# Optimization experiments

Hardware: AMD Instinct MI355X
Metric: run time of the kernel (lower is better)

Reference implementation:

```python
import jax, jax.numpy as jnp
import numpy as np

MODEL_DIM = 768
EMB_DIM = 768
NUM_HEADS = 12
HEAD_DIM = MODEL_DIM // NUM_HEADS  # 64
B, S = 4, 1024
LN_EPS = 1e-12


def setup_inputs() -> dict:
    key = jax.random.key(0)
    ks = jax.random.split(key, 12)
    s_in = 1.0 / np.sqrt(EMB_DIM)
    s_dm = 1.0 / np.sqrt(MODEL_DIM)
    return {
        "x": jax.random.normal(ks[0], (B, S, EMB_DIM), dtype=jnp.float32),
        # stacked per-head projection weights, [H, E, Dh] (in, out layout)
        "Wq": jax.random.normal(ks[1], (NUM_HEADS, EMB_DIM, HEAD_DIM), dtype=jnp.float32) * s_in,
        "bq": jax.random.normal(ks[2], (NUM_HEADS, HEAD_DIM), dtype=jnp.float32) * 0.02,
        "Wk": jax.random.normal(ks[3], (NUM_HEADS, EMB_DIM, HEAD_DIM), dtype=jnp.float32) * s_in,
        "bk": jax.random.normal(ks[4], (NUM_HEADS, HEAD_DIM), dtype=jnp.float32) * 0.02,
        "Wv": jax.random.normal(ks[5], (NUM_HEADS, EMB_DIM, HEAD_DIM), dtype=jnp.float32) * s_in,
        "bv": jax.random.normal(ks[6], (NUM_HEADS, HEAD_DIM), dtype=jnp.float32) * 0.02,
        # output dense [Dm, Dm] (in, out) + bias
        "Wd": jax.random.normal(ks[7], (MODEL_DIM, MODEL_DIM), dtype=jnp.float32) * s_dm,
        "bd": jax.random.normal(ks[8], (MODEL_DIM,), dtype=jnp.float32) * 0.02,
        # LayerNorm affine params
        "gamma": jnp.ones((MODEL_DIM,), dtype=jnp.float32),
        "beta": jnp.zeros((MODEL_DIM,), dtype=jnp.float32),
    }


def reference(x, Wq, bq, Wk, bk, Wv, bv, Wd, bd, gamma, beta):
    # Batched per-head projections: [B,S,E] x [H,E,Dh] -> [B,H,S,Dh]
    Q = jnp.einsum("bse,hed->bhsd", x, Wq) + bq[None, :, None, :]
    K = jnp.einsum("bse,hed->bhsd", x, Wk) + bk[None, :, None, :]
    V = jnp.einsum("bse,hed->bhsd", x, Wv) + bv[None, :, None, :]

    scale = 1.0 / jnp.sqrt(jnp.asarray(HEAD_DIM, dtype=Q.dtype))
    scores = jnp.einsum("bhsd,bhtd->bhst", Q, K) * scale  # [B,H,S,S]
    weights = jax.nn.softmax(scores, axis=-1)
    ctx = jnp.einsum("bhst,bhtd->bhsd", weights, V)  # [B,H,S,Dh]

    # concat per-head outputs along last dim (head order): [B,S,H*Dh]
    outputs = jnp.transpose(ctx, (0, 2, 1, 3)).reshape(B, S, NUM_HEADS * HEAD_DIM)
    # concat per-head attention weights along last dim: [B,S,H*S]
    weights_cat = jnp.transpose(weights, (0, 2, 1, 3)).reshape(B, S, NUM_HEADS * S)

    # BertSelfOutput: dense -> LayerNorm (dropout = identity in eval)
    y = jnp.einsum("bsi,io->bso", outputs, Wd) + bd
    mu = jnp.mean(y, axis=-1, keepdims=True)
    var = jnp.mean(jnp.square(y - mu), axis=-1, keepdims=True)
    y = (y - mu) * jax.lax.rsqrt(var + LN_EPS) * gamma + beta
    return weights_cat, y
```

## Files before the change

### kernel.cpp

```cpp
#include <hip/hip_runtime.h>

typedef __bf16 bf16x8 __attribute__((ext_vector_type(8)));
typedef float  f32x4  __attribute__((ext_vector_type(4)));
typedef unsigned short u16x8 __attribute__((ext_vector_type(8)));
typedef unsigned short u16x4 __attribute__((ext_vector_type(4)));

__device__ __forceinline__ unsigned short f2bf(float f) {
  union { float f; unsigned u; } v; v.f = f;
  unsigned r = v.u + 0x7fffu + ((v.u >> 16) & 1u);
  return (unsigned short)(r >> 16);
}

__device__ __forceinline__ float bf2f(unsigned short b) {
  union { unsigned u; float f; } v; v.u = (unsigned)b << 16;
  return v.f;
}

__device__ __forceinline__ void gload16(const unsigned short* g, unsigned short* l) {
  __builtin_amdgcn_global_load_lds(
      (const __attribute__((address_space(1))) unsigned int*)g,
      (__attribute__((address_space(3))) unsigned int*)l,
      16, 0, 0);
}

__device__ __forceinline__ void nt_store4(float* p, f32x4 v) {
  __builtin_nontemporal_store(v, (f32x4*)p);
}

#define WOFF 50331648

__device__ __forceinline__ int eidx(int row, int col) {
  return row * 1024 + ((((col >> 3) ^ (row & 7)) << 3) | (col & 7));
}

__global__ __launch_bounds__(256) void prep(
    const float* __restrict__ x, const float* __restrict__ Wq, const float* __restrict__ Wk,
    const float* __restrict__ Wv, const float* __restrict__ Wd,
    unsigned short* __restrict__ xb, unsigned short* __restrict__ wb, unsigned short* __restrict__ wdb)
{
  __shared__ float t[32][33];
  const int bid = blockIdx.x, tid = threadIdx.x;
  if (bid < 1536) {
    int i = (bid * 256 + tid) * 8;
    f32x4 v0 = *(const f32x4*)&x[i];
    f32x4 v1 = *(const f32x4*)&x[i + 4];
    u16x8 o;
    for (int j = 0; j < 4; j++) { o[j] = f2bf(v0[j]); o[j + 4] = f2bf(v1[j]); }
    *(u16x8*)&xb[i] = o;
    return;
  }
  const int tx = tid & 31, ty = tid >> 5;
  if (bid < 3264) {
    int q = bid - 1536;
    int bx = q & 1; q >>= 1;
    int by = q % 24, zz = q / 24;
    int m = zz / 12;
    const float* in = (m == 0 ? Wq : m == 1 ? Wk : Wv) + (long)(zz % 12) * 49152;
    unsigned short* ob = wb + (long)zz * 49152;
    int c = bx * 32 + tx, r0 = by * 32;
    for (int i = ty; i < 32; i += 8) t[i][tx] = in[(long)(r0 + i) * 64 + c];
    __syncthreads();
    int c0 = bx * 32;
    for (int i = ty; i < 32; i += 8) ob[(long)(c0 + i) * 768 + r0 + tx] = f2bf(t[tx][i]);
    return;
  }
  {
    int q = bid - 3264;
    int bx = q % 24, by = q / 24;
    int c = bx * 32 + tx, r0 = by * 32;
    for (int i = ty; i < 32; i += 8) t[i][tx] = Wd[(long)(r0 + i) * 768 + c];
    __syncthreads();
    int c0 = bx * 32;
    for (int i = ty; i < 32; i += 8) wdb[(long)(c0 + i) * 768 + r0 + tx] = f2bf(t[tx][i]);
  }
}

__global__ __launch_bounds__(256) void qkv_gemm(
    const unsigned short* __restrict__ xb, const unsigned short* __restrict__ wb,
    const float* __restrict__ bq, const float* __restrict__ bk, const float* __restrict__ bv,
    unsigned short* __restrict__ Qb, unsigned short* __restrict__ Kb, unsigned short* __restrict__ Vt)
{
  __shared__ unsigned short As[2][4096];
  __shared__ unsigned short Bs[2][4096];
  const int tid = threadIdx.x;
  const int bid = blockIdx.x;
  const int swz = (bid & 7) * 72 + (bid >> 3);
  const int bn = (swz % 18) * 128, bm = (swz / 18) * 128;
  const int w = tid >> 6, l = tid & 63;
  const int wr = w >> 1, wc = w & 1;
  const int lr = l & 15, lg = l >> 4;
  const int lofs = w << 9;

  f32x4 acc[4][4];
  for (int i = 0; i < 4; i++) for (int j = 0; j < 4; j++) acc[i][j] = {0.f, 0.f, 0.f, 0.f};

  const unsigned short* ga = xb + (long)(bm + (tid >> 2)) * 768 + (tid & 3) * 8;
  const unsigned short* gb = wb + (long)(bn + (tid >> 2)) * 768 + (tid & 3) * 8;

  gload16(ga,            &As[0][lofs]);
  gload16(ga + 64 * 768, &As[0][lofs + 2048]);
  gload16(gb,            &Bs[0][lofs]);
  gload16(gb + 64 * 768, &Bs[0][lofs + 2048]);
  __syncthreads();

  int cur = 0;
  for (int t = 0; t < 24; t++) {
    if (t < 23) {
      int k0 = (t + 1) * 32;
      gload16(ga + k0,            &As[cur ^ 1][lofs]);
      gload16(ga + k0 + 64 * 768, &As[cur ^ 1][lofs + 2048]);
      gload16(gb + k0,            &Bs[cur ^ 1][lofs]);
      gload16(gb + k0 + 64 * 768, &Bs[cur ^ 1][lofs + 2048]);
    }
    bf16x8 af[4], bfv[4];
    for (int i = 0; i < 4; i++) af[i]  = *(const bf16x8*)&As[cur][(wr * 64 + i * 16 + lr) * 32 + lg * 8];
    for (int j = 0; j < 4; j++) bfv[j] = *(const bf16x8*)&Bs[cur][(wc * 64 + j * 16 + lr) * 32 + lg * 8];
    for (int i = 0; i < 4; i++)
      for (int j = 0; j < 4; j++)
        acc[i][j] = __builtin_amdgcn_mfma_f32_16x16x32_bf16(af[i], bfv[j], acc[i][j], 0, 0, 0);
    __syncthreads();
    cur ^= 1;
  }

  for (int i = 0; i < 4; i++) for (int j = 0; j < 4; j++) {
    int col = bn + wc * 64 + j * 16 + lr;
    int m = col / 768, rc = col % 768;
    int h = rc >> 6, d = rc & 63;
    const float* bias = (m == 0) ? bq : (m == 1) ? bk : bv;
    float bb = bias[rc];
    for (int r = 0; r < 4; r++) {
      int row = bm + wr * 64 + i * 16 + lg * 4 + r;
      int b = row >> 10, s = row & 1023;
      float v = acc[i][j][r] + bb;
      if (m == 0)      Qb[((b * 12 + h) << 16) + (s << 6) + d] = f2bf(v * 0.125f);
      else if (m == 1) Kb[((b * 12 + h) << 16) + (s << 6) + d] = f2bf(v);
      else             Vt[((b * 12 + h) << 16) + (d << 10) + s] = f2bf(v);
    }
  }
}

__global__ __launch_bounds__(512) void attn_kernel(
    const unsigned short* __restrict__ Qb, const unsigned short* __restrict__ Kb,
    const unsigned short* __restrict__ Vt,
    float* __restrict__ wout, unsigned short* __restrict__ ctx)
{
  extern __shared__ char smem[];
  unsigned short* E  = (unsigned short*)smem;
  unsigned short* Qs = (unsigned short*)(smem + 65536);
  float* sred = (float*)(smem + 70144);
  float* sfin = (float*)(smem + 71168);

  const int bid = blockIdx.x;
  const int swz = (bid & 7) * 192 + (bid >> 3);
  const int bh = swz >> 5;
  const int q0 = (swz & 31) * 32;
  const int b = bh / 12, h = bh % 12;
  const int tid = threadIdx.x;
  const int w = tid >> 6, l = tid & 63, lr = l & 15, lg = l >> 4;
  const unsigned short* Qg = Qb + (bh << 16);
  const unsigned short* Kg = Kb + (bh << 16);
  const unsigned short* Vg = Vt + (bh << 16);

  if (tid < 256) {
    int row = tid >> 3, c = (tid & 7) * 8;
    *(u16x8*)&Qs[row * 72 + c] = *(const u16x8*)&Qg[(q0 + row) * 64 + c];
  }
  __syncthreads();

  bf16x8 qa[2][2];
  for (int ri = 0; ri < 2; ri++) {
    qa[ri][0] = *(const bf16x8*)&Qs[(ri * 16 + lr) * 72 + lg * 8];
    qa[ri][1] = *(const bf16x8*)&Qs[(ri * 16 + lr) * 72 + 32 + lg * 8];
  }
  f32x4 sc[2][8];
#pragma unroll
  for (int cf = 0; cf < 8; cf++) {
    int colb = w * 128 + cf * 16;
    bf16x8 kb0 = *(const bf16x8*)&Kg[(colb + lr) * 64 + lg * 8];
    bf16x8 kb1 = *(const bf16x8*)&Kg[(colb + lr) * 64 + 32 + lg * 8];
#pragma unroll
    for (int ri = 0; ri < 2; ri++) {
      f32x4 a = {0.f, 0.f, 0.f, 0.f};
      a = __builtin_amdgcn_mfma_f32_16x16x32_bf16(qa[ri][0], kb0, a, 0, 0, 0);
      a = __builtin_amdgcn_mfma_f32_16x16x32_bf16(qa[ri][1], kb1, a, 0, 0, 0);
      sc[ri][cf] = a;
    }
  }

  float sm[2][4] = {{0.f, 0.f, 0.f, 0.f}, {0.f, 0.f, 0.f, 0.f}};
#pragma unroll
  for (int cf = 0; cf < 8; cf++)
#pragma unroll
    for (int ri = 0; ri < 2; ri++)
#pragma unroll
      for (int r = 0; r < 4; r++) {
        float e = __expf(sc[ri][cf][r]);
        sm[ri][r] += e;
        E[eidx(ri * 16 + lg * 4 + r, w * 128 + cf * 16 + lr)] = f2bf(e);
      }
#pragma unroll
  for (int ri = 0; ri < 2; ri++)
#pragma unroll
    for (int r = 0; r < 4; r++) {
      float s = sm[ri][r];
      for (int o = 8; o >= 1; o >>= 1) s += __shfl_xor(s, o, 16);
      if (lr == 0) sred[w * 32 + ri * 16 + lg * 4 + r] = s;
    }
  __syncthreads();

  if (tid < 32) {
    float s = 0.f;
    for (int ww = 0; ww < 8; ww++) s += sred[ww * 32 + tid];
    sfin[tid] = 1.f / s;
  }

  int ri = w >> 2, cf = w & 3;
  f32x4 acc = {0.f, 0.f, 0.f, 0.f};
#pragma unroll
  for (int ks = 0; ks < 32; ks++) {
    int kk = ks * 32;
    bf16x8 pa = *(const bf16x8*)&E[eidx(ri * 16 + lr, kk + lg * 8)];
    bf16x8 vb = *(const bf16x8*)&Vg[(cf * 16 + lr) * 1024 + kk + lg * 8];
    acc = __builtin_amdgcn_mfma_f32_16x16x32_bf16(pa, vb, acc, 0, 0, 0);
  }
  __syncthreads();

#pragma unroll
  for (int r = 0; r < 4; r++) {
    int row = ri * 16 + lg * 4 + r;
    float v = acc[r] * sfin[row];
    ctx[(long)(b * 1024 + q0 + row) * 768 + h * 64 + cf * 16 + lr] = f2bf(v);
  }

  {
    float* wbase = wout + (long)(b * 1024 + q0) * 12288 + h * 1024;
#pragma unroll
    for (int it = 0; it < 16; it++) {
      int vidx = it * 512 + tid;
      int row = vidx >> 8, c4 = (vidx & 255) * 4;
      float rs = sfin[row];
      u16x4 ev = *(const u16x4*)&E[eidx(row, c4)];
      f32x4 o;
      for (int t = 0; t < 4; t++) o[t] = bf2f(ev[t]) * rs;
      *(f32x4*)&wbase[(long)row * 12288 + c4] = o;
    }
  }
}

__global__ __launch_bounds__(256) void dense_gemm(
    const unsigned short* __restrict__ ctx, const unsigned short* __restrict__ wdb,
    const float* __restrict__ bd, float* __restrict__ y)
{
  __shared__ unsigned short As[2][2048];
  __shared__ unsigned short Bs[2][4096];
  const int tid = threadIdx.x;
  const int bid = blockIdx.x;
  const int swz = (bid & 7) * 48 + (bid >> 3);
  const int bn = (swz % 6) * 128, bm = (swz / 6) * 64;
  const int w = tid >> 6, l = tid & 63;
  const int wr = w >> 1, wc = w & 1;
  const int lr = l & 15, lg = l >> 4;
  const int lofs = w << 9;

  f32x4 acc[2][4];
  for (int i = 0; i < 2; i++) for (int j = 0; j < 4; j++) acc[i][j] = {0.f, 0.f, 0.f, 0.f};

  const unsigned short* ga = ctx + (long)(bm + (tid >> 2)) * 768 + (tid & 3) * 8;
  const unsigned short* gb = wdb + (long)(bn + (tid >> 2)) * 768 + (tid & 3) * 8;

  gload16(ga,            &As[0][lofs]);
  gload16(gb,            &Bs[0][lofs]);
  gload16(gb + 64 * 768, &Bs[0][lofs + 2048]);
  __syncthreads();

  int cur = 0;
  for (int t = 0; t < 24; t++) {
    if (t < 23) {
      int k0 = (t + 1) * 32;
      gload16(ga + k0,            &As[cur ^ 1][lofs]);
      gload16(gb + k0,            &Bs[cur ^ 1][lofs]);
      gload16(gb + k0 + 64 * 768, &Bs[cur ^ 1][lofs + 2048]);
    }
    bf16x8 af[2], bfv[4];
    for (int i = 0; i < 2; i++) af[i]  = *(const bf16x8*)&As[cur][(wr * 32 + i * 16 + lr) * 32 + lg * 8];
    for (int j = 0; j < 4; j++) bfv[j] = *(const bf16x8*)&Bs[cur][(wc * 64 + j * 16 + lr) * 32 + lg * 8];
    for (int i = 0; i < 2; i++)
      for (int j = 0; j < 4; j++)
        acc[i][j] = __builtin_amdgcn_mfma_f32_16x16x32_bf16(af[i], bfv[j], acc[i][j], 0, 0, 0);
    __syncthreads();
    cur ^= 1;
  }

  for (int i = 0; i < 2; i++) for (int j = 0; j < 4; j++) {
    int col = bn + wc * 64 + j * 16 + lr;
    float bb = bd[col];
    for (int r = 0; r < 4; r++) {
      int row = bm + wr * 32 + i * 16 + lg * 4 + r;
      y[(long)row * 768 + col] = acc[i][j][r] + bb;
    }
  }
}

__global__ __launch_bounds__(256) void ln_kernel(
    const float* __restrict__ y,
    const float* __restrict__ gamma, const float* __restrict__ beta,
    float* __restrict__ out)
{
  int w = threadIdx.x >> 6, l = threadIdx.x & 63;
  long row = blockIdx.x * 4 + w;
  const float* yr = y + row * 768;
  f32x4 v[3];
  float s = 0.f, ss = 0.f;
  for (int j = 0; j < 3; j++) {
    int c = j * 256 + l * 4;
    f32x4 t = *(const f32x4*)&yr[c];
    for (int q = 0; q < 4; q++) { s += t[q]; ss += t[q] * t[q]; }
    v[j] = t;
  }
  for (int o = 32; o >= 1; o >>= 1) { s += __shfl_xor(s, o); ss += __shfl_xor(ss, o); }
  float mu = s * (1.f / 768.f);
  float var = ss * (1.f / 768.f) - mu * mu;
  float rs = rsqrtf(var + 1e-12f);
  float* orow = out + row * 768;
  for (int j = 0; j < 3; j++) {
    int c = j * 256 + l * 4;
    f32x4 g = *(const f32x4*)&gamma[c];
    f32x4 be = *(const f32x4*)&beta[c];
    f32x4 o;
    for (int q = 0; q < 4; q++) o[q] = (v[j][q] - mu) * rs * g[q] + be[q];
    nt_store4(&orow[c], o);
  }
}

extern "C" void kernel_launch(void* const* d_in, const int* in_sizes, int n_in,
                              void* d_out, int out_size, void* d_ws, size_t ws_size,
                              hipStream_t stream) {
  const float* x     = (const float*)d_in[0];
  const float* Wq    = (const float*)d_in[1];
  const float* bq    = (const float*)d_in[2];
  const float* Wk    = (const float*)d_in[3];
  const float* bk    = (const float*)d_in[4];
  const float* Wv    = (const float*)d_in[5];
  const float* bv    = (const float*)d_in[6];
  const float* Wd    = (const float*)d_in[7];
  const float* bd    = (const float*)d_in[8];
  const float* gamma = (const float*)d_in[9];
  const float* beta  = (const float*)d_in[10];
  float* out = (float*)d_out;

  char* ws = (char*)d_ws;
  unsigned short* xb  = (unsigned short*)(ws);
  unsigned short* wb  = (unsigned short*)(ws + 6291456);
  unsigned short* wdb = (unsigned short*)(ws + 9830400);
  unsigned short* Qb  = (unsigned short*)(ws + 11010048);
  unsigned short* Kb  = (unsigned short*)(ws + 17301504);
  unsigned short* Vt  = (unsigned short*)(ws + 23592960);
  unsigned short* ctx = (unsigned short*)(ws + 29884416);
  float*          yws = (float*)(ws + 11010048);

  prep<<<3840, 256, 0, stream>>>(x, Wq, Wk, Wv, Wd, xb, wb, wdb);
  qkv_gemm<<<576, 256, 0, stream>>>(xb, wb, bq, bk, bv, Qb, Kb, Vt);
  attn_kernel<<<1536, 512, 71296, stream>>>(Qb, Kb, Vt, out, ctx);
  dense_gemm<<<384, 256, 0, stream>>>(ctx, wdb, bd, yws);
  ln_kernel<<<1024, 256, 0, stream>>>(yws, gamma, beta, out + WOFF);
}
```

Baseline: 156.1 us.

## Split attention waves into PV-MFMA and weight-store groups, drop Q LDS staging

Q fragments are now loaded straight from global memory, which removes the Q shared-memory buffer and one barrier. Every wave now computes the row-sum reciprocals itself from sred, so the serial single-thread reduction and its sfin buffer are gone. The post-softmax work is split by wave: waves 0-3 run the P·V MFMAs at raised priority, while waves 4-7 write the normalized fp32 attention weights. The goal is to overlap compute with the large weight stores and to lower LDS use so more blocks fit per CU, at the cost of half as many waves doing each task.

```diff
diff --git a/kernel.cpp b/kernel.cpp
--- a/kernel.cpp
+++ b/kernel.cpp
@@ -139,16 +139,14 @@
   }
 }
 
-__global__ __launch_bounds__(512) void attn_kernel(
+__global__ __launch_bounds__(512, 4) void attn_kernel(
     const unsigned short* __restrict__ Qb, const unsigned short* __restrict__ Kb,
     const unsigned short* __restrict__ Vt,
     float* __restrict__ wout, unsigned short* __restrict__ ctx)
 {
   extern __shared__ char smem[];
-  unsigned short* E  = (unsigned short*)smem;
-  unsigned short* Qs = (unsigned short*)(smem + 65536);
-  float* sred = (float*)(smem + 70144);
-  float* sfin = (float*)(smem + 71168);
+  unsigned short* E = (unsigned short*)smem;
+  float* sred = (float*)(smem + 65536);
 
   const int bid = blockIdx.x;
   const int swz = (bid & 7) * 192 + (bid >> 3);
@@ -161,17 +159,13 @@
   const unsigned short* Kg = Kb + (bh << 16);
   const unsigned short* Vg = Vt + (bh << 16);
 
-  if (tid < 256) {
-    int row = tid >> 3, c = (tid & 7) * 8;
-    *(u16x8*)&Qs[row * 72 + c] = *(const u16x8*)&Qg[(q0 + row) * 64 + c];
-  }
-  __syncthreads();
-
   bf16x8 qa[2][2];
-  for (int ri = 0; ri < 2; ri++) {
-    qa[ri][0] = *(const bf16x8*)&Qs[(ri * 16 + lr) * 72 + lg * 8];
-    qa[ri][1] = *(const bf16x8*)&Qs[(ri * 16 + lr) * 72 + 32 + lg * 8];
-  }
+#pragma unroll
+  for (int ri = 0; ri < 2; ri++)
+#pragma unroll
+    for (int ks = 0; ks < 2; ks++)
+      qa[ri][ks] = *(const bf16x8*)&Qg[(q0 + ri * 16 + lr) * 64 + ks * 32 + lg * 8];
+
   f32x4 sc[2][8];
 #pragma unroll
   for (int cf = 0; cf < 8; cf++) {
@@ -206,42 +200,50 @@
       for (int o = 8; o >= 1; o >>= 1) s += __shfl_xor(s, o, 16);
       if (lr == 0) sred[w * 32 + ri * 16 + lg * 4 + r] = s;
     }
+
   __syncthreads();
 
-  if (tid < 32) {
-    float s = 0.f;
-    for (int ww = 0; ww < 8; ww++) s += sred[ww * 32 + tid];
-    sfin[tid] = 1.f / s;
-  }
-
-  int ri = w >> 2, cf = w & 3;
-  f32x4 acc = {0.f, 0.f, 0.f, 0.f};
-#pragma unroll
-  for (int ks = 0; ks < 32; ks++) {
-    int kk = ks * 32;
-    bf16x8 pa = *(const bf16x8*)&E[eidx(ri * 16 + lr, kk + lg * 8)];
-    bf16x8 vb = *(const bf16x8*)&Vg[(cf * 16 + lr) * 1024 + kk + lg * 8];
-    acc = __builtin_amdgcn_mfma_f32_16x16x32_bf16(pa, vb, acc, 0, 0, 0);
-  }
-  __syncthreads();
-
-#pragma unroll
-  for (int r = 0; r < 4; r++) {
-    int row = ri * 16 + lg * 4 + r;
-    float v = acc[r] * sfin[row];
-    ctx[(long)(b * 1024 + q0 + row) * 768 + h * 64 + cf * 16 + lr] = f2bf(v);
-  }
-
+  float s_acc = 0.f;
   {
+    int row_l = l & 31;
+#pragma unroll
+    for (int ww = 0; ww < 8; ww++) s_acc += sred[ww * 32 + row_l];
+  }
+  const float sfin_r = 1.f / s_acc;
+
+  if (w < 4) {
+    const int ri = w >> 1, cfp = (w & 1) * 2;
+    f32x4 acc0 = {0.f, 0.f, 0.f, 0.f};
+    f32x4 acc1 = {0.f, 0.f, 0.f, 0.f};
+    __builtin_amdgcn_s_setprio(1);
+#pragma unroll
+    for (int ks = 0; ks < 32; ks++) {
+      int kk = ks * 32;
+      bf16x8 pa  = *(const bf16x8*)&E[eidx(ri * 16 + lr, kk + lg * 8)];
+      bf16x8 vb0 = *(const bf16x8*)&Vg[(cfp * 16 + lr) * 1024 + kk + lg * 8];
+      bf16x8 vb1 = *(const bf16x8*)&Vg[((cfp + 1) * 16 + lr) * 1024 + kk + lg * 8];
+      acc0 = __builtin_amdgcn_mfma_f32_16x16x32_bf16(pa, vb0, acc0, 0, 0, 0);
+      acc1 = __builtin_amdgcn_mfma_f32_16x16x32_bf16(pa, vb1, acc1, 0, 0, 0);
+    }
+    __builtin_amdgcn_s_setprio(0);
+#pragma unroll
+    for (int r = 0; r < 4; r++) {
+      int row = ri * 16 + lg * 4 + r;
+      float sf = __shfl(sfin_r, row);
+      long base = (long)(b * 1024 + q0 + row) * 768 + h * 64;
+      ctx[base + cfp * 16 + lr]       = f2bf(acc0[r] * sf);
+      ctx[base + (cfp + 1) * 16 + lr] = f2bf(acc1[r] * sf);
+    }
+  } else {
+    const int t = tid - 256;
     float* wbase = wout + (long)(b * 1024 + q0) * 12288 + h * 1024;
 #pragma unroll
-    for (int it = 0; it < 16; it++) {
-      int vidx = it * 512 + tid;
-      int row = vidx >> 8, c4 = (vidx & 255) * 4;
-      float rs = sfin[row];
+    for (int row = 0; row < 32; row++) {
+      float sf = __shfl(sfin_r, row);
+      int c4 = t * 4;
       u16x4 ev = *(const u16x4*)&E[eidx(row, c4)];
       f32x4 o;
-      for (int t = 0; t < 4; t++) o[t] = bf2f(ev[t]) * rs;
+      for (int j = 0; j < 4; j++) o[j] = bf2f(ev[j]) * sf;
       *(f32x4*)&wbase[(long)row * 12288 + c4] = o;
     }
   }
@@ -360,7 +362,7 @@
 
   prep<<<3840, 256, 0, stream>>>(x, Wq, Wk, Wv, Wd, xb, wb, wdb);
   qkv_gemm<<<576, 256, 0, stream>>>(xb, wb, bq, bk, bv, Qb, Kb, Vt);
-  attn_kernel<<<1536, 512, 71296, stream>>>(Qb, Kb, Vt, out, ctx);
+  attn_kernel<<<1536, 512, 66560, stream>>>(Qb, Kb, Vt, out, ctx);
   dense_gemm<<<384, 256, 0, stream>>>(ctx, wdb, bd, yws);
   ln_kernel<<<1024, 256, 0, stream>>>(yws, gamma, beta, out + WOFF);
 }
```

New measurement: 155.3 us. Within noise of the previous version (-0.5%).
